# Kernel optimization log

Hardware: AMD Instinct MI355X
Metric: run time of the kernel (lower is better)

Reference implementation:

```python
import jax, jax.numpy as jnp
import numpy as np

N_NODES = 50000
N_EDGES = 1600000
IN_CH = 256
LAT = 32
HID = 64
OUT_CH = 256
GAT_H = 32  # GAT hidden dims [32, 32], heads=1


def setup_inputs() -> dict:
    key = jax.random.key(0)
    ks = jax.random.split(key, 30)
    nrm = lambda k, shape, s=0.05: jax.random.normal(k, shape, dtype=jnp.float32) * s
    inp = {}
    inp["x"] = jax.random.normal(ks[0], (N_NODES, IN_CH), dtype=jnp.float32)
    inp["edge_index"] = jax.random.randint(ks[1], (2, N_EDGES), 0, N_NODES)
    # GAT layer 1: IN_CH -> 32 (heads=1), layer 2: 32 -> 32, final linear 32 -> LAT
    inp["W_g1"] = nrm(ks[2], (IN_CH, GAT_H)); inp["as_g1"] = nrm(ks[3], (GAT_H,)); inp["ad_g1"] = nrm(ks[4], (GAT_H,)); inp["b_g1"] = jnp.zeros((GAT_H,), jnp.float32)
    inp["W_g2"] = nrm(ks[5], (GAT_H, GAT_H)); inp["as_g2"] = nrm(ks[6], (GAT_H,)); inp["ad_g2"] = nrm(ks[7], (GAT_H,)); inp["b_g2"] = jnp.zeros((GAT_H,), jnp.float32)
    inp["W_gf"] = nrm(ks[8], (GAT_H, LAT)); inp["b_gf"] = jnp.zeros((LAT,), jnp.float32)
    inp["W_m1"] = nrm(ks[9], (IN_CH, HID)); inp["b_m1"] = jnp.zeros((HID,), jnp.float32); inp["g_m1"] = jnp.ones((HID,), jnp.float32); inp["be_m1"] = jnp.zeros((HID,), jnp.float32)
    inp["W_m2"] = nrm(ks[10], (HID, HID)); inp["b_m2"] = jnp.zeros((HID,), jnp.float32); inp["g_m2"] = jnp.ones((HID,), jnp.float32); inp["be_m2"] = jnp.zeros((HID,), jnp.float32)
    inp["W_m3"] = nrm(ks[11], (HID, LAT)); inp["b_m3"] = jnp.zeros((LAT,), jnp.float32); inp["g_m3"] = jnp.ones((LAT,), jnp.float32); inp["be_m3"] = jnp.zeros((LAT,), jnp.float32)
    # final linear LAT -> OUT_CH + ReLU
    inp["W_f"] = nrm(ks[12], (LAT, OUT_CH)); inp["b_f"] = jnp.zeros((OUT_CH,), jnp.float32)
    return inp


def _bn_relu(h, g, b):
    # BatchNorm1d in training mode: batch stats, biased variance, eps=1e-5
    m = jnp.mean(h, axis=0)
    v = jnp.var(h, axis=0)
    return jax.nn.relu((h - m) * jax.lax.rsqrt(v + 1e-5) * g + b)


def _gat(h_in, src, dst, W, a_s, a_d, b):
    # PyG GATConv (heads=1): edge (src j -> dst i), e = LeakyReLU(a_src.Wx_j + a_dst.Wx_i)
    N = h_in.shape[0]
    h = h_in @ W                                   # [N, F]
    e = jax.nn.leaky_relu((h @ a_s)[src] + (h @ a_d)[dst], 0.2)  # [E]
    m = jax.ops.segment_max(e, dst, num_segments=N)              # scatter-softmax over incoming edges
    ex = jnp.exp(e - m[dst])
    den = jax.ops.segment_sum(ex, dst, num_segments=N)
    alpha = ex / den[dst]
    out = jax.ops.segment_sum(alpha[:, None] * h[src], dst, num_segments=N)
    return out + b


def reference(x, edge_index, W_g1, as_g1, ad_g1, b_g1, W_g2, as_g2, ad_g2, b_g2, W_gf, b_gf, W_m1, b_m1, g_m1, be_m1, W_m2, b_m2, g_m2, be_m2, W_m3, b_m3, g_m3, be_m3, W_f, b_f):
    N = x.shape[0]
    loops = jnp.arange(N)
    src = jnp.concatenate([edge_index[0], loops])  # PyG add_self_loops=True
    dst = jnp.concatenate([edge_index[1], loops])
    r = _bn_relu(x @ W_m1 + b_m1, g_m1, be_m1)
    r = _bn_relu(r @ W_m2 + b_m2, g_m2, be_m2)
    r = _bn_relu(r @ W_m3 + b_m3, g_m3, be_m3)
    # GAT interpolation branch (dropout inactive in eval)
    h = jax.nn.relu(_gat(x, src, dst, W_g1, as_g1, ad_g1, b_g1))
    h = jax.nn.relu(_gat(h, src, dst, W_g2, as_g2, ad_g2, b_g2))
    h = h @ W_gf + b_gf
    # blend with alphas = 0.5 constant vector
    out = 0.5 * r + 0.5 * h
    return jax.nn.relu(out @ W_f + b_f)
```

## Files before the change

kernel.cpp:

```cpp
#include <hip/hip_runtime.h>

#define NNODES 50000
#define NEDGES 1600000
#define NBUCK 196
#define BIN_CH 4096
#define CNT_CH 4096

typedef __attribute__((ext_vector_type(4))) float f32x4;
typedef __attribute__((ext_vector_type(8))) short short8;

__device__ __forceinline__ float leaky02(float x) { return x > 0.f ? x : 0.2f * x; }

__device__ __forceinline__ int block_incl_scan(int v, int* sh) {
  int t = threadIdx.x;
  sh[t] = v;
  __syncthreads();
  for (int d = 1; d < 256; d <<= 1) {
    int u = (t >= d) ? sh[t - d] : 0;
    __syncthreads();
    sh[t] += u;
    __syncthreads();
  }
  return sh[t];
}

__global__ __launch_bounds__(256) void k_b0(const int* __restrict__ dst,
                                            int* __restrict__ gcnt, int E) {
  __shared__ int hist[256];
  int t = threadIdx.x;
  hist[t] = 0;
  __syncthreads();
  int base0 = blockIdx.x * CNT_CH;
#pragma unroll
  for (int r = 0; r < CNT_CH / 256; ++r) {
    int idx = base0 + r * 256 + t;
    if (idx < E) atomicAdd(&hist[dst[idx] >> 8], 1);
  }
  __syncthreads();
  if (t < NBUCK && hist[t]) atomicAdd(&gcnt[t], hist[t]);
}

__global__ __launch_bounds__(256) void k_b1(const int* __restrict__ gcnt,
                                            int* __restrict__ base,
                                            int* __restrict__ cursor) {
  __shared__ int sh[256];
  int t = threadIdx.x;
  int v = (t < NBUCK) ? gcnt[t] : 0;
  int incl = block_incl_scan(v, sh);
  if (t < NBUCK) {
    base[t] = incl - v;
    cursor[t] = incl - v;
  }
  if (t == 255) base[NBUCK] = NEDGES;
}

__global__ __launch_bounds__(256) void k_bin(const int* __restrict__ src,
                                             const int* __restrict__ dst,
                                             int* __restrict__ cursor,
                                             unsigned* __restrict__ binned, int E) {
  __shared__ int hist[256];
  __shared__ int cur[256];
  int t = threadIdx.x;
  int base0 = blockIdx.x * BIN_CH;
  unsigned pk[BIN_CH / 256];
  hist[t] = 0;
  __syncthreads();
#pragma unroll
  for (int r = 0; r < BIN_CH / 256; ++r) {
    int idx = base0 + r * 256 + t;
    if (idx < E) {
      unsigned p = ((unsigned)dst[idx] << 16) | (unsigned)src[idx];
      pk[r] = p;
      atomicAdd(&hist[p >> 24], 1);
    }
  }
  __syncthreads();
  if (t < NBUCK && hist[t]) cur[t] = atomicAdd(&cursor[t], hist[t]);
  __syncthreads();
#pragma unroll
  for (int r = 0; r < BIN_CH / 256; ++r) {
    int idx = base0 + r * 256 + t;
    if (idx < E) {
      unsigned p = pk[r];
      int pos = atomicAdd(&cur[p >> 24], 1);
      binned[pos] = p;
    }
  }
}

__global__ __launch_bounds__(256) void k_sort(const unsigned* __restrict__ binned,
                                              const int* __restrict__ base,
                                              int* __restrict__ deg,
                                              int* __restrict__ offs,
                                              int* __restrict__ csr) {
  __shared__ int hist[256];
  __shared__ int scanbuf[256];
  __shared__ int cur[256];
  int t = threadIdx.x;
  int b = blockIdx.x;
  int lo = base[b], hi = base[b + 1];
  int node0 = b << 8;
  hist[t] = 0;
  __syncthreads();
  for (int i = lo + t; i < hi; i += 256)
    atomicAdd(&hist[(binned[i] >> 16) & 255], 1);
  __syncthreads();
  int h = hist[t];
  int incl = block_incl_scan(h, scanbuf);
  int excl = incl - h;
  int node = node0 + t;
  if (node < NNODES) {
    deg[node] = h;
    offs[node] = lo + excl;
  }
  cur[t] = lo + excl;
  __syncthreads();
  for (int i = lo + t; i < hi; i += 256) {
    unsigned p = binned[i];
    int pos = atomicAdd(&cur[(p >> 16) & 255], 1);
    csr[pos] = (int)(p & 0xFFFFu);
  }
}

template <int K, int NC, int TN, int SPLIT, bool BN, bool STATS, int ROWS>
__global__ __launch_bounds__(256) void k_gemm(
    const float* __restrict__ A, const float* __restrict__ bn_sum,
    const float* __restrict__ bn_sq, const float* __restrict__ bn_gamma,
    const float* __restrict__ bn_beta, float invM,
    const float* __restrict__ B0, const float* __restrict__ B1,
    const float* __restrict__ bias0,
    float* __restrict__ out0, float* __restrict__ out1,
    float* __restrict__ gsum, float* __restrict__ gsq, int M) {
  constexpr int KC = 64;
  constexpr int RPT = ROWS / 16;
  __shared__ float As[ROWS * KC];
  __shared__ float Bs[KC * NC];
  __shared__ float scS[BN ? K : 4];
  __shared__ float shS[BN ? K : 4];
  const int tid = threadIdx.x;
  const int row0 = blockIdx.x * ROWS;
  const int cg = tid & 15;
  const int rowg = (tid >> 4) & 15;
  const int swz = (rowg & 3) << 2;

  if constexpr (BN) {
    if (tid < K) {
      float mean = bn_sum[tid] * invM;
      float var = bn_sq[tid] * invM - mean * mean;
      float rs = rsqrtf(var + 1e-5f);
      float sc = rs * bn_gamma[tid];
      scS[tid] = sc;
      shS[tid] = bn_beta[tid] - mean * sc;
    }
    __syncthreads();
  }

  float acc[RPT][TN];
#pragma unroll
  for (int r = 0; r < RPT; ++r)
#pragma unroll
    for (int j = 0; j < TN; ++j) acc[r][j] = 0.f;

  constexpr int KB = KC / 4;
  for (int k0 = 0; k0 < K; k0 += KC) {
#pragma unroll
    for (int it = 0; it < (ROWS * KB) / 256; ++it) {
      int idx = tid + it * 256;
      int row = idx / KB;
      int kb = idx % KB;
      float4 v = make_float4(0.f, 0.f, 0.f, 0.f);
      int grow = row0 + row;
      if (grow < M) {
        v = *reinterpret_cast<const float4*>(&A[(size_t)grow * K + k0 + kb * 4]);
        if constexpr (BN) {
          int kb4 = k0 + kb * 4;
          float4 sc = *reinterpret_cast<const float4*>(&scS[kb4]);
          float4 sf = *reinterpret_cast<const float4*>(&shS[kb4]);
          v.x = fmaxf(v.x * sc.x + sf.x, 0.f);
          v.y = fmaxf(v.y * sc.y + sf.y, 0.f);
          v.z = fmaxf(v.z * sc.z + sf.z, 0.f);
          v.w = fmaxf(v.w * sc.w + sf.w, 0.f);
        }
      }
      *reinterpret_cast<float4*>(&As[row * KC + ((kb ^ (row & 3)) * 4)]) = v;
    }
    {
      constexpr int KB0 = SPLIT / 4;
#pragma unroll
      for (int it = 0; it < (KC * KB0) / 256; ++it) {
        int idx = tid + it * 256;
        int kk = idx / KB0;
        int cb = idx % KB0;
        float4 v = *reinterpret_cast<const float4*>(&B0[(size_t)(k0 + kk) * SPLIT + cb * 4]);
        *reinterpret_cast<float4*>(&Bs[kk * NC + cb * 4]) = v;
      }
    }
    if constexpr (NC > SPLIT) {
      constexpr int W1 = NC - SPLIT;
      constexpr int KB1 = W1 / 4;
#pragma unroll
      for (int it = 0; it < (KC * KB1) / 256; ++it) {
        int idx = tid + it * 256;
        int kk = idx / KB1;
        int cb = idx % KB1;
        float4 v = *reinterpret_cast<const float4*>(&B1[(size_t)(k0 + kk) * W1 + cb * 4]);
        *reinterpret_cast<float4*>(&Bs[kk * NC + SPLIT + cb * 4]) = v;
      }
    }
    __syncthreads();
    for (int kk = 0; kk < KC; kk += 4) {
      float4 a[RPT];
#pragma unroll
      for (int r = 0; r < RPT; ++r)
        a[r] = *reinterpret_cast<const float4*>(&As[(rowg + 16 * r) * KC + (kk ^ swz)]);
      float b[4][TN];
#pragma unroll
      for (int i = 0; i < 4; ++i)
#pragma unroll
        for (int j = 0; j < TN; ++j) b[i][j] = Bs[(kk + i) * NC + cg * TN + j];
#pragma unroll
      for (int r = 0; r < RPT; ++r)
#pragma unroll
        for (int j = 0; j < TN; ++j) {
          acc[r][j] += a[r].x * b[0][j];
          acc[r][j] += a[r].y * b[1][j];
          acc[r][j] += a[r].z * b[2][j];
          acc[r][j] += a[r].w * b[3][j];
        }
    }
    __syncthreads();
  }
  float bias_r[TN];
#pragma unroll
  for (int j = 0; j < TN; ++j) {
    int c = cg * TN + j;
    bias_r[j] = (c < SPLIT) ? bias0[c] : 0.f;
  }
  float cs[TN], cq[TN];
#pragma unroll
  for (int j = 0; j < TN; ++j) { cs[j] = 0.f; cq[j] = 0.f; }
#pragma unroll
  for (int r = 0; r < RPT; ++r) {
    int grow = row0 + rowg + 16 * r;
    if (grow < M) {
#pragma unroll
      for (int j = 0; j < TN; ++j) {
        int c = cg * TN + j;
        if (c < SPLIT) {
          float v = acc[r][j] + bias_r[j];
          out0[(size_t)grow * SPLIT + c] = v;
          if (STATS) { cs[j] += v; cq[j] += v * v; }
        } else {
          out1[(size_t)grow * (NC - SPLIT) + (c - SPLIT)] = acc[r][j];
        }
      }
    }
  }
  if constexpr (STATS) {
#pragma unroll
    for (int j = 0; j < TN; ++j) {
      cs[j] += __shfl_xor(cs[j], 16);
      cs[j] += __shfl_xor(cs[j], 32);
      cq[j] += __shfl_xor(cq[j], 16);
      cq[j] += __shfl_xor(cq[j], 32);
    }
    float* red = Bs;
    int wave = tid >> 6;
    int lane = tid & 63;
    if (lane < 16) {
#pragma unroll
      for (int j = 0; j < TN; ++j) {
        int c = cg * TN + j;
        if (c < SPLIT) {
          red[wave * 2 * SPLIT + c] = cs[j];
          red[wave * 2 * SPLIT + SPLIT + c] = cq[j];
        }
      }
    }
    __syncthreads();
    if (tid < SPLIT) {
      float s = red[tid] + red[2 * SPLIT + tid] + red[4 * SPLIT + tid] + red[6 * SPLIT + tid];
      atomicAdd(&gsum[tid], s);
    } else if (tid < 2 * SPLIT) {
      int c = tid - SPLIT;
      float q = red[SPLIT + c] + red[3 * SPLIT + c] + red[5 * SPLIT + c] + red[7 * SPLIT + c];
      atomicAdd(&gsq[c], q);
    }
  }
}

__global__ __launch_bounds__(512) void k_bsplit(const float* __restrict__ Wm,
                                                const float* __restrict__ Wg,
                                                unsigned short* __restrict__ Bt) {
  int b = blockIdx.x;
  int cc = b / 6, cf = b % 6;
  int t = threadIdx.x;
  int lane = t >> 3, j = t & 7;
  int lg = lane >> 4, lc = lane & 15;
  int k = cc * 32 + lg * 8 + j;
  int col = cf * 16 + lc;
  float v = (col < 64) ? Wm[k * 64 + col] : Wg[k * 32 + (col - 64)];
  unsigned bb = __float_as_uint(v);
  unsigned h = bb & 0xffff0000u;
  float lo = v - __uint_as_float(h);
  Bt[(size_t)(b * 2 + 0) * 512 + t] = (unsigned short)(h >> 16);
  Bt[(size_t)(b * 2 + 1) * 512 + t] = (unsigned short)(__float_as_uint(lo) >> 16);
}

__global__ __launch_bounds__(512) void k_bsplit2(const float* __restrict__ Wf,
                                                 unsigned short* __restrict__ WfT) {
  int cf = blockIdx.x;
  int t = threadIdx.x;
  int lane = t >> 3, j = t & 7;
  int lg = lane >> 4, lc = lane & 15;
  int k = lg * 8 + j;
  int col = cf * 16 + lc;
  float v = Wf[k * 256 + col];
  unsigned bb = __float_as_uint(v);
  unsigned h = bb & 0xffff0000u;
  float lo = v - __uint_as_float(h);
  WfT[(size_t)(cf * 2 + 0) * 512 + t] = (unsigned short)(h >> 16);
  WfT[(size_t)(cf * 2 + 1) * 512 + t] = (unsigned short)(__float_as_uint(lo) >> 16);
}

union U16 { uint4 u; short8 s; };
__device__ __forceinline__ short8 as_s8(uint4 u) { U16 t; t.u = u; return t.s; }

__device__ __forceinline__ void split2(float x0, float x1, unsigned& h, unsigned& l) {
  unsigned b0 = __float_as_uint(x0), b1 = __float_as_uint(x1);
  unsigned h0 = b0 & 0xffff0000u, h1 = b1 & 0xffff0000u;
  h = (h0 >> 16) | h1;
  float l0 = x0 - __uint_as_float(h0);
  float l1 = x1 - __uint_as_float(h1);
  l = (__float_as_uint(l0) >> 16) | (__float_as_uint(l1) & 0xffff0000u);
}

__device__ __forceinline__ void split8(const float4& a, const float4& b,
                                       short8& hi, short8& lo) {
  uint4 h, l;
  split2(a.x, a.y, h.x, l.x);
  split2(a.z, a.w, h.y, l.y);
  split2(b.x, b.y, h.z, l.z);
  split2(b.z, b.w, h.w, l.w);
  hi = as_s8(h);
  lo = as_s8(l);
}

__device__ __forceinline__ void gload16(const void* g, void* l) {
  __builtin_amdgcn_global_load_lds(
      (const __attribute__((address_space(1))) void*)g,
      (__attribute__((address_space(3))) void*)l, 16, 0, 0);
}

__global__ __launch_bounds__(256) void k_gemm1_mfma(
    const float* __restrict__ A, const unsigned short* __restrict__ Bt,
    const float* __restrict__ bias0,
    float* __restrict__ out0, float* __restrict__ out1,
    float* __restrict__ gsum, float* __restrict__ gsq, int M) {
  __shared__ float As[2][64 * 32];
  __shared__ __align__(16) unsigned short Bs[2][6144];
  __shared__ float red[512];
  const int tid = threadIdx.x;
  const int wv = tid >> 6;
  const int lane = tid & 63;
  const int lg = lane >> 4;
  const int lc = lane & 15;
  const int wr = wv >> 1;
  const int wc = wv & 1;
  const int rowb = blockIdx.x * 64;

  const int srow = lane >> 3;
  const int sfetch = (lane & 7) ^ srow;

  const int rl0 = wr * 32 + lc;
  const int rl1 = rl0 + 16;

  f32x4 acc[2][3];
#pragma unroll
  for (int rf = 0; rf < 2; ++rf)
#pragma unroll
    for (int j = 0; j < 3; ++j) acc[rf][j] = (f32x4){0.f, 0.f, 0.f, 0.f};

#pragma unroll
  for (int q = 0; q < 2; ++q) {
    int lrow = wv * 16 + q * 8 + srow;
    int grow = rowb + lrow;
    grow = grow < M ? grow : M - 1;
    gload16(A + (size_t)grow * 256 + sfetch * 4, &As[0][(wv * 16 + q * 8) * 32]);
  }
#pragma unroll
  for (int i = 0; i < 3; ++i) {
    int off = (wv * 3 + i) * 1024;
    gload16((const char*)Bt + off + lane * 16, (char*)Bs[0] + off);
  }
  __syncthreads();

#pragma unroll
  for (int c = 0; c < 8; ++c) {
    const int buf = c & 1;
    if (c < 7) {
#pragma unroll
      for (int q = 0; q < 2; ++q) {
        int lrow = wv * 16 + q * 8 + srow;
        int grow = rowb + lrow;
        grow = grow < M ? grow : M - 1;
        gload16(A + (size_t)grow * 256 + (c + 1) * 32 + sfetch * 4,
                &As[buf ^ 1][(wv * 16 + q * 8) * 32]);
      }
#pragma unroll
      for (int i = 0; i < 3; ++i) {
        int off = (wv * 3 + i) * 1024;
        gload16((const char*)Bt + (size_t)(c + 1) * 12288 + off + lane * 16,
                (char*)Bs[buf ^ 1] + off);
      }
    }
    uint4 bhr[3], blr[3];
#pragma unroll
    for (int j = 0; j < 3; ++j) {
      const unsigned short* bp = &Bs[buf][((wc * 3 + j) * 2) * 512 + lane * 8];
      bhr[j] = *reinterpret_cast<const uint4*>(bp);
      blr[j] = *reinterpret_cast<const uint4*>(bp + 512);
    }
    float4 a00 = *reinterpret_cast<const float4*>(
        &As[buf][rl0 * 32 + ((2 * lg) ^ (rl0 & 7)) * 4]);
    float4 a01 = *reinterpret_cast<const float4*>(
        &As[buf][rl0 * 32 + ((2 * lg + 1) ^ (rl0 & 7)) * 4]);
    float4 a10 = *reinterpret_cast<const float4*>(
        &As[buf][rl1 * 32 + ((2 * lg) ^ (rl1 & 7)) * 4]);
    float4 a11 = *reinterpret_cast<const float4*>(
        &As[buf][rl1 * 32 + ((2 * lg + 1) ^ (rl1 & 7)) * 4]);
    short8 ah0, al0, ah1, al1;
    split8(a00, a01, ah0, al0);
    split8(a10, a11, ah1, al1);
#pragma unroll
    for (int j = 0; j < 3; ++j) {
      short8 bh = as_s8(bhr[j]), bl = as_s8(blr[j]);
      acc[0][j] = __builtin_amdgcn_mfma_f32_16x16x32_bf16(ah0, bh, acc[0][j], 0, 0, 0);
      acc[0][j] = __builtin_amdgcn_mfma_f32_16x16x32_bf16(al0, bh, acc[0][j], 0, 0, 0);
      acc[0][j] = __builtin_amdgcn_mfma_f32_16x16x32_bf16(ah0, bl, acc[0][j], 0, 0, 0);
      acc[1][j] = __builtin_amdgcn_mfma_f32_16x16x32_bf16(ah1, bh, acc[1][j], 0, 0, 0);
      acc[1][j] = __builtin_amdgcn_mfma_f32_16x16x32_bf16(al1, bh, acc[1][j], 0, 0, 0);
      acc[1][j] = __builtin_amdgcn_mfma_f32_16x16x32_bf16(ah1, bl, acc[1][j], 0, 0, 0);
    }
    __syncthreads();
  }

  red[tid] = 0.f;
  red[tid + 256] = 0.f;
  __syncthreads();

  float bias_r[3];
#pragma unroll
  for (int j = 0; j < 3; ++j) {
    int gcf = wc * 3 + j;
    bias_r[j] = (gcf < 4) ? bias0[gcf * 16 + lc] : 0.f;
  }
  float cs[3] = {0.f, 0.f, 0.f}, cq[3] = {0.f, 0.f, 0.f};
#pragma unroll
  for (int rf = 0; rf < 2; ++rf) {
    int rbase = rowb + wr * 32 + rf * 16 + lg * 4;
#pragma unroll
    for (int i = 0; i < 4; ++i) {
      int row = rbase + i;
      if (row < M) {
#pragma unroll
        for (int j = 0; j < 3; ++j) {
          int gcf = wc * 3 + j;
          if (gcf < 4) {
            float v = acc[rf][j][i] + bias_r[j];
            out0[(size_t)row * 64 + gcf * 16 + lc] = v;
            cs[j] += v;
            cq[j] += v * v;
          } else {
            out1[(size_t)row * 32 + (gcf - 4) * 16 + lc] = acc[rf][j][i];
          }
        }
      }
    }
  }
#pragma unroll
  for (int j = 0; j < 3; ++j) {
    cs[j] += __shfl_xor(cs[j], 16);
    cs[j] += __shfl_xor(cs[j], 32);
    cq[j] += __shfl_xor(cq[j], 16);
    cq[j] += __shfl_xor(cq[j], 32);
  }
  if (lg == 0) {
#pragma unroll
    for (int j = 0; j < 3; ++j) {
      int gcf = wc * 3 + j;
      if (gcf < 4) {
        red[wv * 128 + gcf * 16 + lc] = cs[j];
        red[wv * 128 + 64 + gcf * 16 + lc] = cq[j];
      }
    }
  }
  __syncthreads();
  if (tid < 64) {
    atomicAdd(&gsum[tid], red[tid] + red[128 + tid] + red[256 + tid] + red[384 + tid]);
  } else if (tid < 128) {
    int cc2 = tid - 64;
    atomicAdd(&gsq[cc2], red[64 + cc2] + red[192 + cc2] + red[320 + cc2] + red[448 + cc2]);
  }
}

__global__ __launch_bounds__(256) void k_sdot(const float* __restrict__ g,
                                              const float* __restrict__ as_,
                                              const float* __restrict__ ad_,
                                              float* __restrict__ sv,
                                              float* __restrict__ dv, int N) {
  int lane = threadIdx.x & 31;
  int row = blockIdx.x * 8 + (threadIdx.x >> 5);
  if (row >= N) return;
  float v = g[(size_t)row * 32 + lane];
  float a = v * as_[lane];
  float b = v * ad_[lane];
#pragma unroll
  for (int w = 16; w >= 1; w >>= 1) {
    a += __shfl_xor(a, w);
    b += __shfl_xor(b, w);
  }
  if (lane == 0) {
    sv[row] = a;
    dv[row] = b;
  }
}

__global__ __launch_bounds__(256) void k_gat_agg(
    const float* __restrict__ h, const float* __restrict__ sv,
    const float* __restrict__ dv, const int* __restrict__ offs,
    const int* __restrict__ deg, const int* __restrict__ csr,
    const float* __restrict__ bias, float* __restrict__ out, int N) {
  int lane = threadIdx.x & 31;
  int node = blockIdx.x * 8 + (threadIdx.x >> 5);
  if (node >= N) return;
  int start = offs[node];
  int cnt = deg[node];
  float di = dv[node];
  float ex0 = __expf(leaky02(sv[node] + di));
  float den = ex0;
  float acc = ex0 * h[(size_t)node * 32 + lane];
  int k = 0;
  for (; k + 8 <= cnt; k += 8) {
    int j0 = csr[start + k + 0], j1 = csr[start + k + 1];
    int j2 = csr[start + k + 2], j3 = csr[start + k + 3];
    int j4 = csr[start + k + 4], j5 = csr[start + k + 5];
    int j6 = csr[start + k + 6], j7 = csr[start + k + 7];
    float s0 = sv[j0], s1 = sv[j1], s2 = sv[j2], s3 = sv[j3];
    float s4 = sv[j4], s5 = sv[j5], s6 = sv[j6], s7 = sv[j7];
    float h0 = h[(size_t)j0 * 32 + lane], h1 = h[(size_t)j1 * 32 + lane];
    float h2 = h[(size_t)j2 * 32 + lane], h3 = h[(size_t)j3 * 32 + lane];
    float h4 = h[(size_t)j4 * 32 + lane], h5 = h[(size_t)j5 * 32 + lane];
    float h6 = h[(size_t)j6 * 32 + lane], h7 = h[(size_t)j7 * 32 + lane];
    float e0 = __expf(leaky02(s0 + di)), e1 = __expf(leaky02(s1 + di));
    float e2 = __expf(leaky02(s2 + di)), e3 = __expf(leaky02(s3 + di));
    float e4 = __expf(leaky02(s4 + di)), e5 = __expf(leaky02(s5 + di));
    float e6 = __expf(leaky02(s6 + di)), e7 = __expf(leaky02(s7 + di));
    den += ((e0 + e1) + (e2 + e3)) + ((e4 + e5) + (e6 + e7));
    acc += e0 * h0 + e1 * h1 + e2 * h2 + e3 * h3;
    acc += e4 * h4 + e5 * h5 + e6 * h6 + e7 * h7;
  }
  for (; k < cnt; ++k) {
    int j = csr[start + k];
    float ex = __expf(leaky02(sv[j] + di));
    den += ex;
    acc += ex * h[(size_t)j * 32 + lane];
  }
  out[(size_t)node * 32 + lane] = fmaxf(acc / den + bias[lane], 0.f);
}

__global__ __launch_bounds__(256) void k_small_gemm_sd(
    const float* __restrict__ hin, const float* __restrict__ W,
    const float* __restrict__ as_, const float* __restrict__ ad_,
    float* __restrict__ gout, float* __restrict__ sv, float* __restrict__ dv,
    int N) {
  __shared__ float Ws[32][32];
  {
    int t = threadIdx.x;
#pragma unroll
    for (int r = 0; r < 4; ++r) {
      int idx = t + r * 256;
      Ws[idx >> 5][idx & 31] = W[idx];
    }
  }
  __syncthreads();
  int lane = threadIdx.x & 31;
  int row = blockIdx.x * 8 + (threadIdx.x >> 5);
  if (row >= N) return;
  float hv = hin[(size_t)row * 32 + lane];
  float acc = 0.f;
#pragma unroll
  for (int k = 0; k < 32; ++k) acc += __shfl(hv, k, 32) * Ws[k][lane];
  gout[(size_t)row * 32 + lane] = acc;
  float a = acc * as_[lane];
  float b = acc * ad_[lane];
#pragma unroll
  for (int w = 16; w >= 1; w >>= 1) {
    a += __shfl_xor(a, w);
    b += __shfl_xor(b, w);
  }
  if (lane == 0) {
    sv[row] = a;
    dv[row] = b;
  }
}

__global__ __launch_bounds__(256) void k_final2(
    const float* __restrict__ mlp3, const float* __restrict__ sum3,
    const float* __restrict__ sq3, const float* __restrict__ g3,
    const float* __restrict__ be3, float invM, const float* __restrict__ h2,
    const float* __restrict__ Wgf, const float* __restrict__ bgf,
    const unsigned short* __restrict__ WfT, const float* __restrict__ bf,
    float* __restrict__ out, int N) {
  __shared__ __align__(16) unsigned short WfS[16384];
  __shared__ float Bl[64][36];
  __shared__ float WgfS[32][33];
  __shared__ float colS[3][32];
  __shared__ float bfS[256];
  __shared__ __align__(16) unsigned short blAh[4][64][8];
  __shared__ __align__(16) unsigned short blAl[4][64][8];
  const int t = threadIdx.x;
  const int wv = t >> 6;
  const int lane = t & 63;
  const int row0 = blockIdx.x * 64;

  {
    const char* src = (const char*)WfT;
    char* dst = (char*)WfS;
#pragma unroll
    for (int i = 0; i < 8; ++i) {
      int off = (i * 4 + wv) * 1024;
      gload16(src + off + lane * 16, dst + off);
    }
  }
#pragma unroll
  for (int r = 0; r < 4; ++r) {
    int idx = t + r * 256;
    WgfS[idx >> 5][idx & 31] = Wgf[idx];
  }
  bfS[t] = bf[t];
  if (t < 32) {
    float mean = sum3[t] * invM;
    float var = sq3[t] * invM - mean * mean;
    float rs = rsqrtf(var + 1e-5f);
    float sc = rs * g3[t];
    colS[0][t] = sc;
    colS[1][t] = be3[t] - mean * sc;
    colS[2][t] = bgf[t];
  }
#pragma unroll
  for (int r = 0; r < 2; ++r) {
    int idx = t + r * 256;
    int row = idx >> 3;
    int k4 = idx & 7;
    int grow = row0 + row;
    float4 v = make_float4(0.f, 0.f, 0.f, 0.f);
    if (grow < N) v = *reinterpret_cast<const float4*>(&h2[(size_t)grow * 32 + k4 * 4]);
    *reinterpret_cast<float4*>(&Bl[row][k4 * 4]) = v;
  }
  __syncthreads();

  const int col = t & 31;
  const int rb = t >> 5;
  float w[32];
#pragma unroll
  for (int k = 0; k < 32; ++k) w[k] = WgfS[k][col];
  const int lpos = 16 * (col >> 3);
  const int jj = col & 7;
#pragma unroll
  for (int r = 0; r < 8; ++r) {
    int row = rb + 8 * r;
    float a = colS[2][col];
#pragma unroll
    for (int k4 = 0; k4 < 8; ++k4) {
      float4 hv = *reinterpret_cast<const float4*>(&Bl[row][k4 * 4]);
      a += hv.x * w[k4 * 4 + 0] + hv.y * w[k4 * 4 + 1] +
           hv.z * w[k4 * 4 + 2] + hv.w * w[k4 * 4 + 3];
    }
    int grow = row0 + row;
    float pre = (grow < N) ? mlp3[(size_t)grow * 32 + col] : 0.f;
    float rv = fmaxf(pre * colS[0][col] + colS[1][col], 0.f);
    float v = 0.5f * rv + 0.5f * a;
    int rf = row >> 4;
    int l = (row & 15) + lpos;
    unsigned hh = __float_as_uint(v) & 0xffff0000u;
    blAh[rf][l][jj] = (unsigned short)(hh >> 16);
    blAl[rf][l][jj] = (unsigned short)(__float_as_uint(v - __uint_as_float(hh)) >> 16);
  }
  __syncthreads();

  short8 ah = as_s8(*reinterpret_cast<const uint4*>(&blAh[wv][lane][0]));
  short8 al = as_s8(*reinterpret_cast<const uint4*>(&blAl[wv][lane][0]));
  f32x4 acc[16];
#pragma unroll
  for (int cf = 0; cf < 16; ++cf) acc[cf] = (f32x4){0.f, 0.f, 0.f, 0.f};
#pragma unroll
  for (int cf = 0; cf < 16; ++cf) {
    short8 bh = as_s8(*reinterpret_cast<const uint4*>(&WfS[(cf * 2) * 512 + lane * 8]));
    short8 bl_ = as_s8(*reinterpret_cast<const uint4*>(&WfS[(cf * 2 + 1) * 512 + lane * 8]));
    acc[cf] = __builtin_amdgcn_mfma_f32_16x16x32_bf16(ah, bh, acc[cf], 0, 0, 0);
    acc[cf] = __builtin_amdgcn_mfma_f32_16x16x32_bf16(al, bh, acc[cf], 0, 0, 0);
    acc[cf] = __builtin_amdgcn_mfma_f32_16x16x32_bf16(ah, bl_, acc[cf], 0, 0, 0);
  }
  const int lg = lane >> 4, lc = lane & 15;
#pragma unroll
  for (int cf = 0; cf < 16; ++cf) {
    float bb = bfS[cf * 16 + lc];
#pragma unroll
    for (int i = 0; i < 4; ++i) {
      int row = row0 + wv * 16 + lg * 4 + i;
      if (row < N)
        out[(size_t)row * 256 + cf * 16 + lc] = fmaxf(acc[cf][i] + bb, 0.f);
    }
  }
}

extern "C" void kernel_launch(void* const* d_in, const int* in_sizes, int n_in,
                              void* d_out, int out_size, void* d_ws, size_t ws_size,
                              hipStream_t stream) {
  const float* x = (const float*)d_in[0];
  const int* edge = (const int*)d_in[1];
  const float* W_g1 = (const float*)d_in[2];
  const float* as_g1 = (const float*)d_in[3];
  const float* ad_g1 = (const float*)d_in[4];
  const float* b_g1 = (const float*)d_in[5];
  const float* W_g2 = (const float*)d_in[6];
  const float* as_g2 = (const float*)d_in[7];
  const float* ad_g2 = (const float*)d_in[8];
  const float* b_g2 = (const float*)d_in[9];
  const float* W_gf = (const float*)d_in[10];
  const float* b_gf = (const float*)d_in[11];
  const float* W_m1 = (const float*)d_in[12];
  const float* b_m1 = (const float*)d_in[13];
  const float* g_m1 = (const float*)d_in[14];
  const float* be_m1 = (const float*)d_in[15];
  const float* W_m2 = (const float*)d_in[16];
  const float* b_m2 = (const float*)d_in[17];
  const float* g_m2 = (const float*)d_in[18];
  const float* be_m2 = (const float*)d_in[19];
  const float* W_m3 = (const float*)d_in[20];
  const float* b_m3 = (const float*)d_in[21];
  const float* g_m3 = (const float*)d_in[22];
  const float* be_m3 = (const float*)d_in[23];
  const float* W_f = (const float*)d_in[24];
  const float* b_f = (const float*)d_in[25];
  float* out = (float*)d_out;

  const int N = NNODES, E = NEDGES;
  const float invM = 1.f / N;
  const int* esrc = edge;
  const int* edst = edge + E;

  float* ws = (float*)d_ws;
  float* g1 = ws;
  float* mlp1 = g1 + (size_t)N * 32;
  float* mlp2 = mlp1 + (size_t)N * 64;
  float* mlp3 = mlp2 + (size_t)N * 64;
  float* h1 = mlp3 + (size_t)N * 32;
  float* g2 = h1 + (size_t)N * 32;
  float* h2 = g2 + (size_t)N * 32;
  float* s1 = h2 + (size_t)N * 32;
  float* d1 = s1 + N;
  float* s2 = d1 + N;
  float* d2 = s2 + N;
  float* stats = d2 + N;
  float* sum1 = stats, *sq1 = stats + 64;
  float* sum2 = stats + 128, *sq2 = stats + 192;
  float* sum3 = stats + 256, *sq3 = stats + 288;
  int* ip = (int*)(stats + 384);
  int* gcnt = ip;
  int* base = gcnt + 256;
  int* cursor = base + 256;
  int* deg = cursor + 256;
  int* offs = deg + N;
  int* csr = offs + N;
  unsigned* binned = (unsigned*)mlp2;
  unsigned short* Bt = (unsigned short*)((char*)mlp2 + (size_t)E * 4);
  unsigned short* WfT = (unsigned short*)(csr + NEDGES);

  hipMemsetAsync(gcnt, 0, 256 * sizeof(int), stream);
  hipMemsetAsync(stats, 0, 384 * sizeof(float), stream);

  k_bsplit<<<48, 512, 0, stream>>>(W_m1, W_g1, Bt);
  k_bsplit2<<<16, 512, 0, stream>>>(W_f, WfT);

  k_b0<<<(E + CNT_CH - 1) / CNT_CH, 256, 0, stream>>>(edst, gcnt, E);
  k_b1<<<1, 256, 0, stream>>>(gcnt, base, cursor);
  k_bin<<<(E + BIN_CH - 1) / BIN_CH, 256, 0, stream>>>(esrc, edst, cursor, binned, E);
  k_sort<<<NBUCK, 256, 0, stream>>>(binned, base, deg, offs, csr);

  const int GB64 = (N + 63) / 64;
  const int GB128 = (N + 127) / 128;

  k_gemm1_mfma<<<GB64, 256, 0, stream>>>(x, Bt, b_m1, mlp1, g1, sum1, sq1, N);
  k_sdot<<<(N + 7) / 8, 256, 0, stream>>>(g1, as_g1, ad_g1, s1, d1, N);
  k_gat_agg<<<(N + 7) / 8, 256, 0, stream>>>(g1, s1, d1, offs, deg, csr, b_g1, h1, N);

  k_gemm<64, 64, 4, 64, true, true, 128><<<GB128, 256, 0, stream>>>(
      mlp1, sum1, sq1, g_m1, be_m1, invM, W_m2, nullptr, b_m2,
      mlp2, nullptr, sum2, sq2, N);

  k_small_gemm_sd<<<(N + 7) / 8, 256, 0, stream>>>(h1, W_g2, as_g2, ad_g2, g2, s2, d2, N);
  k_gat_agg<<<(N + 7) / 8, 256, 0, stream>>>(g2, s2, d2, offs, deg, csr, b_g2, h2, N);

  k_gemm<64, 32, 2, 32, true, true, 128><<<GB128, 256, 0, stream>>>(
      mlp2, sum2, sq2, g_m2, be_m2, invM, W_m3, nullptr, b_m3,
      mlp3, nullptr, sum3, sq3, N);

  k_final2<<<GB64, 256, 0, stream>>>(mlp3, sum3, sq3, g_m3, be_m3, invM,
                                     h2, W_gf, b_gf, WfT, b_f, out, N);
}
```

Measured before the change: 394.5 us.

## Load full A tile to LDS once and read B directly from global

The GEMM1 kernel now stages the entire 64x256 fp32 A tile in LDS with one upfront batch of async loads and a single barrier, replacing the double-buffered per-chunk pipeline. The B operand is read straight from global memory, where it is small and likely cache-resident, instead of being staged in LDS. This removes the per-iteration barriers and the LDS copies of B, and launch bounds now request two blocks per CU. The cost is 64KB of LDS per block, which limits occupancy, and a loss of overlap between the loads and the MFMA work.

```diff
diff --git a/kernel.cpp b/kernel.cpp
--- a/kernel.cpp
+++ b/kernel.cpp
@@ -352,13 +352,12 @@
       (__attribute__((address_space(3))) void*)l, 16, 0, 0);
 }
 
-__global__ __launch_bounds__(256) void k_gemm1_mfma(
+__global__ __launch_bounds__(256, 2) void k_gemm1_mfma(
     const float* __restrict__ A, const unsigned short* __restrict__ Bt,
     const float* __restrict__ bias0,
     float* __restrict__ out0, float* __restrict__ out1,
     float* __restrict__ gsum, float* __restrict__ gsq, int M) {
-  __shared__ float As[2][64 * 32];
-  __shared__ __align__(16) unsigned short Bs[2][6144];
+  __shared__ float As[64 * 256];
   __shared__ float red[512];
   const int tid = threadIdx.x;
   const int wv = tid >> 6;
@@ -369,66 +368,45 @@
   const int wc = wv & 1;
   const int rowb = blockIdx.x * 64;
 
-  const int srow = lane >> 3;
-  const int sfetch = (lane & 7) ^ srow;
+#pragma unroll
+  for (int q = 0; q < 16; ++q) {
+    int lrow = wv * 16 + q;
+    int grow = rowb + lrow;
+    grow = grow < M ? grow : M - 1;
+    int g = (lane & 56) | ((lane & 7) ^ (lrow & 7));
+    gload16(A + (size_t)grow * 256 + g * 4, &As[lrow * 256]);
+  }
+
+  f32x4 acc[2][3];
+#pragma unroll
+  for (int rf = 0; rf < 2; ++rf)
+#pragma unroll
+    for (int j = 0; j < 3; ++j) acc[rf][j] = (f32x4){0.f, 0.f, 0.f, 0.f};
+
+  __syncthreads();
 
   const int rl0 = wr * 32 + lc;
   const int rl1 = rl0 + 16;
-
-  f32x4 acc[2][3];
-#pragma unroll
-  for (int rf = 0; rf < 2; ++rf)
-#pragma unroll
-    for (int j = 0; j < 3; ++j) acc[rf][j] = (f32x4){0.f, 0.f, 0.f, 0.f};
-
-#pragma unroll
-  for (int q = 0; q < 2; ++q) {
-    int lrow = wv * 16 + q * 8 + srow;
-    int grow = rowb + lrow;
-    grow = grow < M ? grow : M - 1;
-    gload16(A + (size_t)grow * 256 + sfetch * 4, &As[0][(wv * 16 + q * 8) * 32]);
-  }
-#pragma unroll
-  for (int i = 0; i < 3; ++i) {
-    int off = (wv * 3 + i) * 1024;
-    gload16((const char*)Bt + off + lane * 16, (char*)Bs[0] + off);
-  }
-  __syncthreads();
+  const int xk = rl0 & 7;
 
 #pragma unroll
   for (int c = 0; c < 8; ++c) {
-    const int buf = c & 1;
-    if (c < 7) {
-#pragma unroll
-      for (int q = 0; q < 2; ++q) {
-        int lrow = wv * 16 + q * 8 + srow;
-        int grow = rowb + lrow;
-        grow = grow < M ? grow : M - 1;
-        gload16(A + (size_t)grow * 256 + (c + 1) * 32 + sfetch * 4,
-                &As[buf ^ 1][(wv * 16 + q * 8) * 32]);
-      }
-#pragma unroll
-      for (int i = 0; i < 3; ++i) {
-        int off = (wv * 3 + i) * 1024;
-        gload16((const char*)Bt + (size_t)(c + 1) * 12288 + off + lane * 16,
-                (char*)Bs[buf ^ 1] + off);
-      }
-    }
     uint4 bhr[3], blr[3];
 #pragma unroll
     for (int j = 0; j < 3; ++j) {
-      const unsigned short* bp = &Bs[buf][((wc * 3 + j) * 2) * 512 + lane * 8];
+      const unsigned short* bp =
+          Bt + (size_t)((c * 6 + wc * 3 + j) * 2) * 512 + lane * 8;
       bhr[j] = *reinterpret_cast<const uint4*>(bp);
       blr[j] = *reinterpret_cast<const uint4*>(bp + 512);
     }
     float4 a00 = *reinterpret_cast<const float4*>(
-        &As[buf][rl0 * 32 + ((2 * lg) ^ (rl0 & 7)) * 4]);
+        &As[rl0 * 256 + (c * 8 + ((2 * lg) ^ xk)) * 4]);
     float4 a01 = *reinterpret_cast<const float4*>(
-        &As[buf][rl0 * 32 + ((2 * lg + 1) ^ (rl0 & 7)) * 4]);
+        &As[rl0 * 256 + (c * 8 + ((2 * lg + 1) ^ xk)) * 4]);
     float4 a10 = *reinterpret_cast<const float4*>(
-        &As[buf][rl1 * 32 + ((2 * lg) ^ (rl1 & 7)) * 4]);
+        &As[rl1 * 256 + (c * 8 + ((2 * lg) ^ xk)) * 4]);
     float4 a11 = *reinterpret_cast<const float4*>(
-        &As[buf][rl1 * 32 + ((2 * lg + 1) ^ (rl1 & 7)) * 4]);
+        &As[rl1 * 256 + (c * 8 + ((2 * lg + 1) ^ xk)) * 4]);
     short8 ah0, al0, ah1, al1;
     split8(a00, a01, ah0, al0);
     split8(a10, a11, ah1, al1);
@@ -442,7 +420,6 @@
       acc[1][j] = __builtin_amdgcn_mfma_f32_16x16x32_bf16(al1, bh, acc[1][j], 0, 0, 0);
       acc[1][j] = __builtin_amdgcn_mfma_f32_16x16x32_bf16(ah1, bl, acc[1][j], 0, 0, 0);
     }
-    __syncthreads();
   }
 
   red[tid] = 0.f;
```

Result: no change. 386.8 us (-2.0%).
